# Kernel tuning notes

Hardware: AMD Instinct MI355X
Metric: run time of the kernel (lower is better)

The kernel has to match this reference:

```python
import jax, jax.numpy as jnp
import numpy as np

B, S, D, H, F = 4, 2048, 1024, 16, 4096
HD = D // H
NEG = -2.0 ** 32
EPS = 1e-5


def _gelu(x):
    return x * 0.5 * (1.0 + jax.scipy.special.erf(x / jnp.sqrt(2.0).astype(x.dtype)))


def _layernorm(x, scale, offset):
    mu = jnp.mean(x, axis=-1, keepdims=True)
    var = jnp.mean(jnp.square(x - mu), axis=-1, keepdims=True)
    return (x - mu) * jax.lax.rsqrt(var + EPS) * scale + offset


def setup_inputs() -> dict:
    key = jax.random.key(0)
    ks = jax.random.split(key, 12)
    s = 0.02
    return {
        "x": jax.random.normal(ks[0], (B, S, D), jnp.float32),
        "mask": jnp.zeros((B, S), jnp.int32),  # 1 = masked-out (padding)
        "Wq": jax.random.normal(ks[1], (D, D), jnp.float32) * s,
        "bq": jnp.zeros((D,), jnp.float32),
        "Wk": jax.random.normal(ks[2], (D, D), jnp.float32) * s,
        "bk": jnp.zeros((D,), jnp.float32),
        "Wv": jax.random.normal(ks[3], (D, D), jnp.float32) * s,
        "bv": jnp.zeros((D,), jnp.float32),
        "Wo": jax.random.normal(ks[4], (D, D), jnp.float32) * s,
        "bo": jnp.zeros((D,), jnp.float32),
        "ln1_s": jnp.ones((D,), jnp.float32),
        "ln1_b": jnp.zeros((D,), jnp.float32),
        "W1": jax.random.normal(ks[5], (D, F), jnp.float32) * s,
        "b1": jnp.zeros((F,), jnp.float32),
        "W2": jax.random.normal(ks[6], (F, D), jnp.float32) * s,
        "b2": jnp.zeros((D,), jnp.float32),
        "ln2_s": jnp.ones((D,), jnp.float32),
        "ln2_b": jnp.zeros((D,), jnp.float32),
    }


def reference(x, mask, Wq, bq, Wk, bk, Wv, bv, Wo, bo, ln1_s, ln1_b,
              W1, b1, W2, b2, ln2_s, ln2_b):
    b, s, d = x.shape
    q = (x @ Wq + bq).reshape(b, s, H, HD)
    k = (x @ Wk + bk).reshape(b, s, H, HD)
    v = (x @ Wv + bv).reshape(b, s, H, HD)
    logits = jnp.einsum('btnh,bsnh->bnts', q, k) / jnp.sqrt(jnp.float32(HD))
    logits = logits + (mask.astype(jnp.float32) * NEG)[:, None, None, :]
    attn = jax.nn.softmax(logits, axis=-1)
    ctx = jnp.einsum('bsnh,bnts->btnh', v, attn).reshape(b, s, d)
    attn_out = ctx @ Wo + bo
    h = _layernorm(attn_out + x, ln1_s, ln1_b)
    mlp = _gelu(h @ W1 + b1) @ W2 + b2
    return _layernorm(mlp + h, ln2_s, ln2_b)
```

## Files before the change

kernel.cpp:

```cpp
#include <hip/hip_runtime.h>
#include <hip/hip_bf16.h>

typedef __attribute__((ext_vector_type(8))) short short8;
typedef __attribute__((ext_vector_type(4))) short s16x4;
typedef __attribute__((ext_vector_type(4))) float f32x4;
typedef unsigned short u16;

#define DEV __device__ __forceinline__
#define MFMA32(a, b, c) __builtin_amdgcn_mfma_f32_16x16x32_bf16(a, b, c, 0, 0, 0)
#define MFMA16(a, b, c) __builtin_amdgcn_mfma_f32_16x16x16bf16_1k(a, b, c, 0, 0, 0)

DEV u16 f2b(float f) {
    __hip_bfloat16 h = __float2bfloat16(f);
    return __builtin_bit_cast(unsigned short, h);
}

DEV float max3f(float a, float b, float c) {
    float d;
    asm("v_max3_f32 %0, %1, %2, %3" : "=v"(d) : "v"(a), "v"(b), "v"(c));
    return d;
}

DEV void gl_lds16(const u16* g, u16* l) {
    __builtin_amdgcn_global_load_lds((const unsigned int*)g, (unsigned int*)l, 16, 0, 0);
}

__global__ __launch_bounds__(256) void cast_bf16(const float* __restrict__ in, u16* __restrict__ out, int n) {
    int i = (blockIdx.x * 256 + threadIdx.x) * 4;
    if (i < n) {
        float4 v = *(const float4*)(in + i);
        ushort4 o;
        o.x = f2b(v.x); o.y = f2b(v.y); o.z = f2b(v.z); o.w = f2b(v.w);
        *(ushort4*)(out + i) = o;
    }
}

__global__ __launch_bounds__(256) void transpose_cast(const float* __restrict__ in, u16* __restrict__ out,
                                                      int R, int C) {
    __shared__ float t[32][33];
    int bx = blockIdx.x * 32;
    int by = blockIdx.y * 32;
    int tx = threadIdx.x, ty = threadIdx.y;
#pragma unroll
    for (int i = 0; i < 32; i += 8) t[ty + i][tx] = in[(size_t)(by + ty + i) * C + bx + tx];
    __syncthreads();
#pragma unroll
    for (int i = 0; i < 32; i += 8) out[(size_t)(bx + ty + i) * R + by + tx] = f2b(t[tx][ty + i]);
}

__global__ __launch_bounds__(256) void pack_bias(const float* __restrict__ bq, const float* __restrict__ bk,
                                                 const float* __restrict__ bv, const float* __restrict__ bo,
                                                 const float* __restrict__ b1, const float* __restrict__ b2,
                                                 float* __restrict__ out) {
    int i = blockIdx.x * 256 + threadIdx.x;
    if (i >= 9216) return;
    float v;
    if (i < 1024) v = bq[i];
    else if (i < 2048) v = bk[i - 1024];
    else if (i < 3072) v = bv[i - 2048];
    else if (i < 4096) v = bo[i - 3072];
    else if (i < 8192) v = b1[i - 4096];
    else v = b2[i - 8192];
    out[i] = v;
}

template <bool GELU, bool BF16OUT>
__global__ __launch_bounds__(256) void gemm_bt(const u16* __restrict__ A, const u16* __restrict__ B,
                                               const float* __restrict__ bias, float* __restrict__ cf,
                                               u16* __restrict__ cb, int M, int N, int K) {
    __shared__ __align__(16) u16 As[128 * 32];
    __shared__ __align__(16) u16 Bs[128 * 32];
    const int tid = threadIdx.x;
    const int wid = tid >> 6, lane = tid & 63;
    const int wr = wid >> 1, wc = wid & 1;
    const int m0 = blockIdx.x * 128, n0 = blockIdx.y * 128;
    const int r16 = lane & 15, g = lane >> 4;
    const int lrow = lane >> 2, lk = (lane & 3) * 8;

    f32x4 acc[4][4];
#pragma unroll
    for (int i = 0; i < 4; i++)
#pragma unroll
        for (int j = 0; j < 4; j++) acc[i][j] = (f32x4){0.f, 0.f, 0.f, 0.f};

    const u16* ga = A + (size_t)(m0 + wid * 32 + lrow) * K + lk;
    const u16* gb = B + (size_t)(n0 + wid * 32 + lrow) * K + lk;
    u16* lA0 = &As[(wid * 32) * 32];
    u16* lA1 = &As[(wid * 32 + 16) * 32];
    u16* lB0 = &Bs[(wid * 32) * 32];
    u16* lB1 = &Bs[(wid * 32 + 16) * 32];

    for (int kt = 0; kt < K; kt += 32) {
        gl_lds16(ga + kt, lA0);
        gl_lds16(ga + (size_t)16 * K + kt, lA1);
        gl_lds16(gb + kt, lB0);
        gl_lds16(gb + (size_t)16 * K + kt, lB1);
        __syncthreads();
        short8 af[4], bfr[4];
#pragma unroll
        for (int i = 0; i < 4; i++) af[i] = *(const short8*)&As[(wr * 64 + i * 16 + r16) * 32 + g * 8];
#pragma unroll
        for (int j = 0; j < 4; j++) bfr[j] = *(const short8*)&Bs[(wc * 64 + j * 16 + r16) * 32 + g * 8];
#pragma unroll
        for (int i = 0; i < 4; i++)
#pragma unroll
            for (int j = 0; j < 4; j++) acc[i][j] = MFMA32(af[i], bfr[j], acc[i][j]);
        __syncthreads();
    }

#pragma unroll
    for (int i = 0; i < 4; i++) {
#pragma unroll
        for (int j = 0; j < 4; j++) {
#pragma unroll
            for (int r = 0; r < 4; r++) {
                int row = m0 + wr * 64 + i * 16 + g * 4 + r;
                int col = n0 + wc * 64 + j * 16 + r16;
                float v = acc[i][j][r] + bias[col];
                if (GELU) v = 0.5f * v * (1.0f + erff(v * 0.70710678118654752f));
                if (BF16OUT) cb[(size_t)row * N + col] = f2b(v);
                else cf[(size_t)row * N + col] = v;
            }
        }
    }
}

__global__ __launch_bounds__(256) void attn_kernel(const u16* __restrict__ qkv, const int* __restrict__ mask,
                                                   u16* __restrict__ ctx) {
    const int tid = threadIdx.x, wid = tid >> 6, lane = tid & 63;
    const int r16 = lane & 15, g = lane >> 4;
    const int h = blockIdx.y, b = blockIdx.z;
    const size_t baserow = (size_t)b * 2048;
    const int q0 = blockIdx.x * 64;

    __shared__ __align__(16) u16 Ks[64 * 64];
    __shared__ __align__(16) u16 Vs[64 * 64];
    __shared__ __align__(16) float mb[64];

    const float SCALE = 0.18033688011112042f;
    const float MNEG = -6.196328018e9f;
    const s16x4 ONES = {(short)0x3F80, (short)0x3F80, (short)0x3F80, (short)0x3F80};

    short8 qf0, qf1;
    {
        const u16* qp = qkv + (baserow + q0 + wid * 16 + r16) * 3072 + h * 64 + g * 8;
        qf0 = *(const short8*)qp;
        qf1 = *(const short8*)(qp + 32);
    }

    const int L = lane;
    const int kchunk = (L & 7) ^ (L >> 3);
    const u16* kg0 = qkv + (baserow + wid * 16 + (L >> 3)) * 3072 + 1024 + h * 64 + kchunk * 8;
    const u16* kg1 = kg0 + (size_t)8 * 3072;
    u16* kl0 = &Ks[wid * 1024];
    u16* kl1 = &Ks[wid * 1024 + 512];
    const u16* vg0 = qkv + (baserow + wid * 16 + ((L & 31) >> 1)) * 3072 + 2048 + h * 64
                     + ((L >> 5) * 16 + (L & 1) * 8);
    const u16* vg1 = vg0 + 32;
    u16* vl0 = &Vs[wid * 1024];
    u16* vl1 = &Vs[wid * 1024 + 512];
    const unsigned vaddr = (unsigned)(unsigned long long)&Vs[0] + (unsigned)(r16 * 2 + g * 128);

    f32x4 Ot[4];
#pragma unroll
    for (int dt = 0; dt < 4; dt++) Ot[dt] = (f32x4){0.f, 0.f, 0.f, 0.f};
    f32x4 Osum = (f32x4){0.f, 0.f, 0.f, 0.f};
    float mrun = -1e30f;

    for (int kt = 0; kt < 2048; kt += 64) {
        const size_t go = (size_t)kt * 3072;
        gl_lds16(kg0 + go, kl0);
        gl_lds16(kg1 + go, kl1);
        gl_lds16(vg0 + go, vl0);
        gl_lds16(vg1 + go, vl1);
        if (tid < 64) mb[tid] = mask[baserow + kt + tid] ? MNEG : 0.0f;
        __syncthreads();

        f32x4 z[4];
        __builtin_amdgcn_s_setprio(1);
#pragma unroll
        for (int t = 0; t < 4; t++) {
            const int row = t * 16 + r16;
            const int swz = row & 7;
            short8 a0 = *(const short8*)&Ks[row * 64 + ((g ^ swz) * 8)];
            short8 a1 = *(const short8*)&Ks[row * 64 + (((4 + g) ^ swz) * 8)];
            f32x4 zz = (f32x4){0.f, 0.f, 0.f, 0.f};
            zz = MFMA32(a0, qf0, zz);
            zz = MFMA32(a1, qf1, zz);
            z[t] = zz;
        }
        __builtin_amdgcn_s_setprio(0);

        f32x4 sv[4];
#pragma unroll
        for (int t = 0; t < 4; t++) {
            f32x4 mbv = *(const f32x4*)&mb[t * 16 + g * 4];
            sv[t] = z[t] * SCALE + mbv;
        }

        float m0 = max3f(sv[0][0], sv[0][1], sv[0][2]);
        float m1 = max3f(sv[0][3], sv[1][0], sv[1][1]);
        float m2 = max3f(sv[1][2], sv[1][3], sv[2][0]);
        float m3 = max3f(sv[2][1], sv[2][2], sv[2][3]);
        float m4 = max3f(sv[3][0], sv[3][1], sv[3][2]);
        float pmax = fmaxf(max3f(m0, m1, m2), max3f(m3, m4, sv[3][3]));
        pmax = fmaxf(pmax, __shfl_xor(pmax, 16));
        pmax = fmaxf(pmax, __shfl_xor(pmax, 32));

        if (!__all(pmax - mrun <= 11.5f)) {
            float mnew = fmaxf(mrun, pmax);
            float alpha = exp2f(mrun - mnew);
            mrun = mnew;
            Osum *= alpha;
#pragma unroll
            for (int dt = 0; dt < 4; dt++) Ot[dt] *= alpha;
        }

        s16x4 pb[4];
#pragma unroll
        for (int t = 0; t < 4; t++) {
            f32x4 d = sv[t] - mrun;
            float p0 = exp2f(d[0]), p1 = exp2f(d[1]), p2 = exp2f(d[2]), p3 = exp2f(d[3]);
            unsigned lo, hi;
            asm("v_cvt_pk_bf16_f32 %0, %1, %2" : "=v"(lo) : "v"(p0), "v"(p1));
            asm("v_cvt_pk_bf16_f32 %0, %1, %2" : "=v"(hi) : "v"(p2), "v"(p3));
            uint2 u; u.x = lo; u.y = hi;
            pb[t] = __builtin_bit_cast(s16x4, u);
        }

        s16x4 vf[4][4];
#pragma unroll
        for (int t = 0; t < 4; t++)
#pragma unroll
            for (int dt = 0; dt < 4; dt++)
                asm volatile("ds_read_b64_tr_b16 %0, %1"
                             : "=v"(vf[t][dt])
                             : "v"(vaddr + (unsigned)((t * 4 + dt) * 512)));
        asm volatile("s_waitcnt lgkmcnt(0)" ::: "memory");
        __builtin_amdgcn_sched_barrier(0);
        __builtin_amdgcn_s_setprio(1);
#pragma unroll
        for (int t = 0; t < 4; t++) {
#pragma unroll
            for (int dt = 0; dt < 4; dt++) Ot[dt] = MFMA16(vf[t][dt], pb[t], Ot[dt]);
            Osum = MFMA16(ONES, pb[t], Osum);
        }
        __builtin_amdgcn_s_setprio(0);
        __syncthreads();
    }

    const float rl = 1.0f / Osum[0];
    u16* cp = ctx + (baserow + q0 + wid * 16 + r16) * 1024 + h * 64 + g * 4;
#pragma unroll
    for (int dt = 0; dt < 4; dt++) {
        ushort4 o4;
        o4.x = f2b(Ot[dt][0] * rl);
        o4.y = f2b(Ot[dt][1] * rl);
        o4.z = f2b(Ot[dt][2] * rl);
        o4.w = f2b(Ot[dt][3] * rl);
        *(ushort4*)(cp + dt * 16) = o4;
    }
}

__global__ __launch_bounds__(256) void ln_kernel(const float* __restrict__ a, const float* __restrict__ res,
                                                 const float* __restrict__ gamma, const float* __restrict__ beta,
                                                 float* __restrict__ outf, u16* __restrict__ outb) {
    const int row = blockIdx.x, tid = threadIdx.x;
    const size_t base = (size_t)row * 1024 + tid * 4;
    float4 va = *(const float4*)(a + base);
    float4 vr = *(const float4*)(res + base);
    float x0 = va.x + vr.x, x1 = va.y + vr.y, x2 = va.z + vr.z, x3 = va.w + vr.w;
    float s = x0 + x1 + x2 + x3;
    float ss = x0 * x0 + x1 * x1 + x2 * x2 + x3 * x3;
#pragma unroll
    for (int m = 1; m < 64; m <<= 1) { s += __shfl_xor(s, m, 64); ss += __shfl_xor(ss, m, 64); }
    __shared__ float red[8];
    if ((tid & 63) == 0) { red[tid >> 6] = s; red[4 + (tid >> 6)] = ss; }
    __syncthreads();
    s = red[0] + red[1] + red[2] + red[3];
    ss = red[4] + red[5] + red[6] + red[7];
    float mu = s * (1.0f / 1024.0f);
    float var = ss * (1.0f / 1024.0f) - mu * mu;
    float rstd = rsqrtf(var + 1e-5f);
    float4 g4 = *(const float4*)(gamma + tid * 4);
    float4 b4 = *(const float4*)(beta + tid * 4);
    float y0 = (x0 - mu) * rstd * g4.x + b4.x;
    float y1 = (x1 - mu) * rstd * g4.y + b4.y;
    float y2 = (x2 - mu) * rstd * g4.z + b4.z;
    float y3 = (x3 - mu) * rstd * g4.w + b4.w;
    *(float4*)(outf + base) = make_float4(y0, y1, y2, y3);
    if (outb) {
        ushort4 ob;
        ob.x = f2b(y0); ob.y = f2b(y1); ob.z = f2b(y2); ob.w = f2b(y3);
        *(ushort4*)(outb + base) = ob;
    }
}

extern "C" void kernel_launch(void* const* d_in, const int* in_sizes, int n_in, void* d_out, int out_size,
                              void* d_ws, size_t ws_size, hipStream_t stream) {
    const float* x = (const float*)d_in[0];
    const int* mask = (const int*)d_in[1];
    const float* Wq = (const float*)d_in[2];
    const float* bq = (const float*)d_in[3];
    const float* Wk = (const float*)d_in[4];
    const float* bk = (const float*)d_in[5];
    const float* Wv = (const float*)d_in[6];
    const float* bv = (const float*)d_in[7];
    const float* Wo = (const float*)d_in[8];
    const float* bo = (const float*)d_in[9];
    const float* ln1s = (const float*)d_in[10];
    const float* ln1b = (const float*)d_in[11];
    const float* W1 = (const float*)d_in[12];
    const float* b1 = (const float*)d_in[13];
    const float* W2 = (const float*)d_in[14];
    const float* b2 = (const float*)d_in[15];
    const float* ln2s = (const float*)d_in[16];
    const float* ln2b = (const float*)d_in[17];
    float* out = (float*)d_out;
    char* ws = (char*)d_ws;

    const size_t MB = 1024 * 1024;
    u16* XB = (u16*)(ws + 0);
    u16* WTq = (u16*)(ws + 16 * MB);
    u16* WTk = WTq + 1024 * 1024;
    u16* WTv = WTk + 1024 * 1024;
    u16* WTo = WTv + 1024 * 1024;
    u16* WT1 = WTo + 1024 * 1024;
    u16* WT2 = WT1 + 4096 * 1024;
    float* BIAS = (float*)(ws + 40 * MB);
    u16* QKV = (u16*)(ws + 41 * MB);
    u16* CTX = (u16*)(ws + 0);
    float* ATT = (float*)(ws + 41 * MB);
    float* Hbuf = (float*)(ws + 73 * MB);
    u16* HB = (u16*)(ws + 105 * MB);
    u16* MLP1 = (u16*)(ws + 121 * MB);
    float* MLP2 = (float*)(ws + 41 * MB);

    dim3 tb(32, 8);
    cast_bf16<<<8192, 256, 0, stream>>>(x, XB, 8192 * 1024);
    transpose_cast<<<dim3(32, 32), tb, 0, stream>>>(Wq, WTq, 1024, 1024);
    transpose_cast<<<dim3(32, 32), tb, 0, stream>>>(Wk, WTk, 1024, 1024);
    transpose_cast<<<dim3(32, 32), tb, 0, stream>>>(Wv, WTv, 1024, 1024);
    transpose_cast<<<dim3(32, 32), tb, 0, stream>>>(Wo, WTo, 1024, 1024);
    transpose_cast<<<dim3(128, 32), tb, 0, stream>>>(W1, WT1, 1024, 4096);
    transpose_cast<<<dim3(32, 128), tb, 0, stream>>>(W2, WT2, 4096, 1024);
    pack_bias<<<36, 256, 0, stream>>>(bq, bk, bv, bo, b1, b2, BIAS);

    gemm_bt<false, true><<<dim3(64, 24), 256, 0, stream>>>(XB, WTq, BIAS, nullptr, QKV, 8192, 3072, 1024);
    attn_kernel<<<dim3(32, 16, 4), 256, 0, stream>>>(QKV, mask, CTX);
    gemm_bt<false, false><<<dim3(64, 8), 256, 0, stream>>>(CTX, WTo, BIAS + 3072, ATT, nullptr, 8192, 1024, 1024);
    ln_kernel<<<8192, 256, 0, stream>>>(ATT, x, ln1s, ln1b, Hbuf, HB);
    gemm_bt<true, true><<<dim3(64, 32), 256, 0, stream>>>(HB, WT1, BIAS + 4096, nullptr, MLP1, 8192, 4096, 1024);
    gemm_bt<false, false><<<dim3(64, 8), 256, 0, stream>>>(MLP1, WT2, BIAS + 8192, MLP2, nullptr, 8192, 1024, 4096);
    ln_kernel<<<8192, 256, 0, stream>>>(MLP2, Hbuf, ln2s, ln2b, out, nullptr);
}
```

Baseline: 529.0 us.

## Double-buffer K/V tiles in attention and fuse residual adds into GEMM epilogues

```diff
diff --git a/kernel.cpp b/kernel.cpp
--- a/kernel.cpp
+++ b/kernel.cpp
@@ -9,6 +9,7 @@
 #define DEV __device__ __forceinline__
 #define MFMA32(a, b, c) __builtin_amdgcn_mfma_f32_16x16x32_bf16(a, b, c, 0, 0, 0)
 #define MFMA16(a, b, c) __builtin_amdgcn_mfma_f32_16x16x16bf16_1k(a, b, c, 0, 0, 0)
+#define SBAR() asm volatile("s_barrier" ::: "memory")
 
 DEV u16 f2b(float f) {
     __hip_bfloat16 h = __float2bfloat16(f);
@@ -64,10 +65,11 @@
     out[i] = v;
 }
 
-template <bool GELU, bool BF16OUT>
+template <bool GELU, bool BF16OUT, bool RESID>
 __global__ __launch_bounds__(256) void gemm_bt(const u16* __restrict__ A, const u16* __restrict__ B,
                                                const float* __restrict__ bias, float* __restrict__ cf,
-                                               u16* __restrict__ cb, int M, int N, int K) {
+                                               u16* __restrict__ cb, const float* __restrict__ res,
+                                               int M, int N, int K) {
     __shared__ __align__(16) u16 As[128 * 32];
     __shared__ __align__(16) u16 Bs[128 * 32];
     const int tid = threadIdx.x;
@@ -117,6 +119,7 @@
                 int row = m0 + wr * 64 + i * 16 + g * 4 + r;
                 int col = n0 + wc * 64 + j * 16 + r16;
                 float v = acc[i][j][r] + bias[col];
+                if (RESID) v += res[(size_t)row * N + col];
                 if (GELU) v = 0.5f * v * (1.0f + erff(v * 0.70710678118654752f));
                 if (BF16OUT) cb[(size_t)row * N + col] = f2b(v);
                 else cf[(size_t)row * N + col] = v;
@@ -133,9 +136,9 @@
     const size_t baserow = (size_t)b * 2048;
     const int q0 = blockIdx.x * 64;
 
-    __shared__ __align__(16) u16 Ks[64 * 64];
-    __shared__ __align__(16) u16 Vs[64 * 64];
-    __shared__ __align__(16) float mb[64];
+    __shared__ __align__(16) u16 Ks[2][64 * 64];
+    __shared__ __align__(16) u16 Vs[2][64 * 64];
+    __shared__ __align__(16) float mb_all[2048];
 
     const float SCALE = 0.18033688011112042f;
     const float MNEG = -6.196328018e9f;
@@ -152,14 +155,18 @@
     const int kchunk = (L & 7) ^ (L >> 3);
     const u16* kg0 = qkv + (baserow + wid * 16 + (L >> 3)) * 3072 + 1024 + h * 64 + kchunk * 8;
     const u16* kg1 = kg0 + (size_t)8 * 3072;
-    u16* kl0 = &Ks[wid * 1024];
-    u16* kl1 = &Ks[wid * 1024 + 512];
     const u16* vg0 = qkv + (baserow + wid * 16 + ((L & 31) >> 1)) * 3072 + 2048 + h * 64
                      + ((L >> 5) * 16 + (L & 1) * 8);
     const u16* vg1 = vg0 + 32;
-    u16* vl0 = &Vs[wid * 1024];
-    u16* vl1 = &Vs[wid * 1024 + 512];
-    const unsigned vaddr = (unsigned)(unsigned long long)&Vs[0] + (unsigned)(r16 * 2 + g * 128);
+    const unsigned vaddr = (unsigned)(unsigned long long)&Vs[0][0] + (unsigned)(r16 * 2 + g * 128);
+
+    for (int i = tid; i < 2048; i += 256) mb_all[i] = mask[baserow + i] ? MNEG : 0.0f;
+
+    gl_lds16(kg0, &Ks[0][wid * 1024]);
+    gl_lds16(kg1, &Ks[0][wid * 1024 + 512]);
+    gl_lds16(vg0, &Vs[0][wid * 1024]);
+    gl_lds16(vg1, &Vs[0][wid * 1024 + 512]);
+    __syncthreads();
 
     f32x4 Ot[4];
 #pragma unroll
@@ -167,35 +174,40 @@
     f32x4 Osum = (f32x4){0.f, 0.f, 0.f, 0.f};
     float mrun = -1e30f;
 
-    for (int kt = 0; kt < 2048; kt += 64) {
-        const size_t go = (size_t)kt * 3072;
-        gl_lds16(kg0 + go, kl0);
-        gl_lds16(kg1 + go, kl1);
-        gl_lds16(vg0 + go, vl0);
-        gl_lds16(vg1 + go, vl1);
-        if (tid < 64) mb[tid] = mask[baserow + kt + tid] ? MNEG : 0.0f;
-        __syncthreads();
+    for (int t = 0; t < 32; ++t) {
+        const int cur = t & 1, nb = cur ^ 1;
+        if (t < 31) {
+            const size_t go = (size_t)(t + 1) * 64 * 3072;
+            gl_lds16(kg0 + go, &Ks[nb][wid * 1024]);
+            gl_lds16(kg1 + go, &Ks[nb][wid * 1024 + 512]);
+            gl_lds16(vg0 + go, &Vs[nb][wid * 1024]);
+            gl_lds16(vg1 + go, &Vs[nb][wid * 1024 + 512]);
+            asm volatile("s_waitcnt vmcnt(4)" ::: "memory");
+        } else {
+            asm volatile("s_waitcnt vmcnt(0)" ::: "memory");
+        }
+        SBAR();
 
         f32x4 z[4];
         __builtin_amdgcn_s_setprio(1);
 #pragma unroll
-        for (int t = 0; t < 4; t++) {
-            const int row = t * 16 + r16;
+        for (int tt = 0; tt < 4; tt++) {
+            const int row = tt * 16 + r16;
             const int swz = row & 7;
-            short8 a0 = *(const short8*)&Ks[row * 64 + ((g ^ swz) * 8)];
-            short8 a1 = *(const short8*)&Ks[row * 64 + (((4 + g) ^ swz) * 8)];
+            short8 a0 = *(const short8*)&Ks[cur][row * 64 + ((g ^ swz) * 8)];
+            short8 a1 = *(const short8*)&Ks[cur][row * 64 + (((4 + g) ^ swz) * 8)];
             f32x4 zz = (f32x4){0.f, 0.f, 0.f, 0.f};
             zz = MFMA32(a0, qf0, zz);
             zz = MFMA32(a1, qf1, zz);
-            z[t] = zz;
+            z[tt] = zz;
         }
         __builtin_amdgcn_s_setprio(0);
 
         f32x4 sv[4];
 #pragma unroll
-        for (int t = 0; t < 4; t++) {
-            f32x4 mbv = *(const f32x4*)&mb[t * 16 + g * 4];
-            sv[t] = z[t] * SCALE + mbv;
+        for (int tt = 0; tt < 4; tt++) {
+            f32x4 mbv = *(const f32x4*)&mb_all[t * 64 + tt * 16 + g * 4];
+            sv[tt] = z[tt] * SCALE + mbv;
         }
 
         float m0 = max3f(sv[0][0], sv[0][1], sv[0][2]);
@@ -218,35 +230,36 @@
 
         s16x4 pb[4];
 #pragma unroll
-        for (int t = 0; t < 4; t++) {
-            f32x4 d = sv[t] - mrun;
+        for (int tt = 0; tt < 4; tt++) {
+            f32x4 d = sv[tt] - mrun;
             float p0 = exp2f(d[0]), p1 = exp2f(d[1]), p2 = exp2f(d[2]), p3 = exp2f(d[3]);
             unsigned lo, hi;
             asm("v_cvt_pk_bf16_f32 %0, %1, %2" : "=v"(lo) : "v"(p0), "v"(p1));
             asm("v_cvt_pk_bf16_f32 %0, %1, %2" : "=v"(hi) : "v"(p2), "v"(p3));
             uint2 u; u.x = lo; u.y = hi;
-            pb[t] = __builtin_bit_cast(s16x4, u);
+            pb[tt] = __builtin_bit_cast(s16x4, u);
         }
 
         s16x4 vf[4][4];
-#pragma unroll
-        for (int t = 0; t < 4; t++)
+        const unsigned va_cur = vaddr + (unsigned)(cur * 8192);
+#pragma unroll
+        for (int tt = 0; tt < 4; tt++)
 #pragma unroll
             for (int dt = 0; dt < 4; dt++)
                 asm volatile("ds_read_b64_tr_b16 %0, %1"
-                             : "=v"(vf[t][dt])
-                             : "v"(vaddr + (unsigned)((t * 4 + dt) * 512)));
+                             : "=v"(vf[tt][dt])
+                             : "v"(va_cur + (unsigned)((tt * 4 + dt) * 512)));
         asm volatile("s_waitcnt lgkmcnt(0)" ::: "memory");
         __builtin_amdgcn_sched_barrier(0);
         __builtin_amdgcn_s_setprio(1);
 #pragma unroll
-        for (int t = 0; t < 4; t++) {
-#pragma unroll
-            for (int dt = 0; dt < 4; dt++) Ot[dt] = MFMA16(vf[t][dt], pb[t], Ot[dt]);
-            Osum = MFMA16(ONES, pb[t], Osum);
+        for (int tt = 0; tt < 4; tt++) {
+#pragma unroll
+            for (int dt = 0; dt < 4; dt++) Ot[dt] = MFMA16(vf[tt][dt], pb[tt], Ot[dt]);
+            Osum = MFMA16(ONES, pb[tt], Osum);
         }
         __builtin_amdgcn_s_setprio(0);
-        __syncthreads();
+        SBAR();
     }
 
     const float rl = 1.0f / Osum[0];
@@ -268,8 +281,11 @@
     const int row = blockIdx.x, tid = threadIdx.x;
     const size_t base = (size_t)row * 1024 + tid * 4;
     float4 va = *(const float4*)(a + base);
-    float4 vr = *(const float4*)(res + base);
-    float x0 = va.x + vr.x, x1 = va.y + vr.y, x2 = va.z + vr.z, x3 = va.w + vr.w;
+    float x0 = va.x, x1 = va.y, x2 = va.z, x3 = va.w;
+    if (res) {
+        float4 vr = *(const float4*)(res + base);
+        x0 += vr.x; x1 += vr.y; x2 += vr.z; x3 += vr.w;
+    }
     float s = x0 + x1 + x2 + x3;
     float ss = x0 * x0 + x1 * x1 + x2 * x2 + x3 * x3;
 #pragma unroll
@@ -346,11 +362,11 @@
     transpose_cast<<<dim3(32, 128), tb, 0, stream>>>(W2, WT2, 4096, 1024);
     pack_bias<<<36, 256, 0, stream>>>(bq, bk, bv, bo, b1, b2, BIAS);
 
-    gemm_bt<false, true><<<dim3(64, 24), 256, 0, stream>>>(XB, WTq, BIAS, nullptr, QKV, 8192, 3072, 1024);
+    gemm_bt<false, true, false><<<dim3(64, 24), 256, 0, stream>>>(XB, WTq, BIAS, nullptr, QKV, nullptr, 8192, 3072, 1024);
     attn_kernel<<<dim3(32, 16, 4), 256, 0, stream>>>(QKV, mask, CTX);
-    gemm_bt<false, false><<<dim3(64, 8), 256, 0, stream>>>(CTX, WTo, BIAS + 3072, ATT, nullptr, 8192, 1024, 1024);
-    ln_kernel<<<8192, 256, 0, stream>>>(ATT, x, ln1s, ln1b, Hbuf, HB);
-    gemm_bt<true, true><<<dim3(64, 32), 256, 0, stream>>>(HB, WT1, BIAS + 4096, nullptr, MLP1, 8192, 4096, 1024);
-    gemm_bt<false, false><<<dim3(64, 8), 256, 0, stream>>>(MLP1, WT2, BIAS + 8192, MLP2, nullptr, 8192, 1024, 4096);
-    ln_kernel<<<8192, 256, 0, stream>>>(MLP2, Hbuf, ln2s, ln2b, out, nullptr);
-}
+    gemm_bt<false, false, true><<<dim3(64, 8), 256, 0, stream>>>(CTX, WTo, BIAS + 3072, ATT, nullptr, x, 8192, 1024, 1024);
+    ln_kernel<<<8192, 256, 0, stream>>>(ATT, nullptr, ln1s, ln1b, Hbuf, HB);
+    gemm_bt<true, true, false><<<dim3(64, 32), 256, 0, stream>>>(HB, WT1, BIAS + 4096, nullptr, MLP1, nullptr, 8192, 4096, 1024);
+    gemm_bt<false, false, true><<<dim3(64, 8), 256, 0, stream>>>(MLP1, WT2, BIAS + 8192, MLP2, nullptr, Hbuf, 8192, 1024, 4096);
+    ln_kernel<<<8192, 256, 0, stream>>>(MLP2, nullptr, ln2s, ln2b, out, nullptr);
+}
```

After: 533.8 us. About the same (+0.9%).
